# Performance work log

Hardware: AMD Instinct MI355X
Metric: run time of the kernel (lower is better)

The kernel has to match this reference:

```python
import jax, jax.numpy as jnp
import numpy as np

N_NODES = 100000


def gcn_conv(x, W, b, src, dst, n_nodes):
    """PyG-style GCNConv: h = D^{-1/2} (A + I) D^{-1/2} (x @ W) + b.

    src/dst already include self-loops. Symmetric normalization with
    degrees computed on the destination index (in-degree incl. self-loop).
    """
    h = x @ W  # [N, out] - transform before propagate (cheap gather dim)
    deg = jax.ops.segment_sum(jnp.ones_like(dst, dtype=h.dtype), dst,
                              num_segments=n_nodes)  # [N]
    dinv = jnp.where(deg > 0, jax.lax.rsqrt(deg), 0.0)  # deg^{-1/2}, 0 for isolated
    norm = dinv[src] * dinv[dst]  # [E]
    msg = h[src] * norm[:, None]  # gather + normalize, [E, out]
    out = jax.ops.segment_sum(msg, dst, num_segments=n_nodes)  # scatter-sum
    return out + b


def setup_inputs() -> dict:
    key = jax.random.key(0)
    k1, k2, k3, k4 = jax.random.split(key, 4)
    in_dim, hidden, n_edges = 128, 32, 3200000
    x = jax.random.normal(k1, (N_NODES, in_dim), dtype=jnp.float32)
    edge_index = jax.random.randint(k2, (2, n_edges), 0, N_NODES, dtype=jnp.int64)
    W1 = jax.random.normal(k3, (in_dim, hidden), dtype=jnp.float32) / np.sqrt(in_dim)
    b1 = jnp.zeros((hidden,), dtype=jnp.float32)
    W2 = jax.random.normal(k4, (hidden, 1), dtype=jnp.float32) / np.sqrt(hidden)
    b2 = jnp.zeros((1,), dtype=jnp.float32)
    return {"x": x, "edge_index": edge_index, "W1": W1, "b1": b1,
            "W2": W2, "b2": b2}


def reference(x, edge_index, W1, b1, W2, b2):
    n = x.shape[0]
    loops = jnp.arange(n, dtype=edge_index.dtype)
    src = jnp.concatenate([edge_index[0], loops])  # add self-loops
    dst = jnp.concatenate([edge_index[1], loops])
    h = jax.nn.relu(gcn_conv(x, W1, b1, src, dst, n))
    out = jax.nn.sigmoid(gcn_conv(h, W2, b2, src, dst, n))
    return out.squeeze(-1)  # [N]
```

## Files before the change

kernel.cpp:

```cpp
#include <hip/hip_runtime.h>
#include <hip/hip_bf16.h>
#include <stdint.h>

#define IN_DIM 128
#define HID 32
#define CSHIFT 8
#define CNODES 256
#define CAP 9216
#define NPART 8
#define SUBCAP 1280
#define TILE 4096
#define NBC_MAX 400

__device__ __forceinline__ float bf_lo(uint u) {
    uint t = u << 16; return *(float*)&t;
}
__device__ __forceinline__ float bf_hi(uint u) {
    uint t = u & 0xFFFF0000u; return *(float*)&t;
}

__global__ __launch_bounds__(256) void binB_kernel(const int* __restrict__ src,
                                                   const int* __restrict__ dst,
                                                   int* __restrict__ pcursor,
                                                   int* __restrict__ pbuf,
                                                   int e, int nbc) {
    __shared__ int pk[TILE];
    __shared__ short binsArr[TILE];
    __shared__ int hist[NBC_MAX];
    __shared__ int gbase[NBC_MAX];
    int part = blockIdx.x & (NPART - 1);
    int base = blockIdx.x * TILE;
    int cnt = min(TILE, e - base);
    if (cnt <= 0) return;
    for (int i = threadIdx.x; i < nbc; i += 256) hist[i] = 0;
    __syncthreads();
    for (int i = threadIdx.x; i < cnt; i += 256) {
        int s = __builtin_nontemporal_load(src + base + i);
        int d = __builtin_nontemporal_load(dst + base + i);
        int bin = d >> CSHIFT;
        pk[i] = s | ((d & (CNODES - 1)) << 17);
        binsArr[i] = (short)bin;
        atomicAdd(&hist[bin], 1);
    }
    __syncthreads();
    for (int i = threadIdx.x; i < nbc; i += 256) {
        int c = hist[i];
        gbase[i] = (c > 0) ? atomicAdd(&pcursor[part * nbc + i], c) : 0;
        hist[i] = 0;
    }
    __syncthreads();
    for (int i = threadIdx.x; i < cnt; i += 256) {
        int bin = binsArr[i];
        int slot = atomicAdd(&hist[bin], 1);
        int pos = gbase[bin] + slot;
        if (pos < SUBCAP)
            pbuf[(size_t)(part * nbc + bin) * SUBCAP + pos] = pk[i];
    }
}

__global__ __launch_bounds__(256) void sortmm_kernel(const int* __restrict__ pcursor,
                                                     const int* __restrict__ pbuf,
                                                     int* __restrict__ csr,
                                                     int* __restrict__ row_beg,
                                                     int* __restrict__ row_end,
                                                     float* __restrict__ dinv_g,
                                                     const float* __restrict__ x,
                                                     const float* __restrict__ W1,
                                                     __hip_bfloat16* __restrict__ h1s,
                                                     int n, int nbc) {
    int b = blockIdx.x;
    __shared__ int sbe[CAP];
    __shared__ int hist[CNODES];
    __shared__ int offs[CNODES];
    __shared__ int cur[CNODES];
    __shared__ int scnt[NPART + 1];
    int tid = threadIdx.x;
    if (tid == 0) {
        int run = 0;
        for (int p = 0; p < NPART; p++) {
            scnt[p] = run;
            run += min(pcursor[p * nbc + b], SUBCAP);
        }
        scnt[NPART] = run;
    }
    hist[tid] = 0;
    __syncthreads();
    for (int p = 0; p < NPART; p++) {
        int cnt = scnt[p + 1] - scnt[p];
        const int* seg = pbuf + (size_t)(p * nbc + b) * SUBCAP;
        int dstoff = scnt[p];
        for (int i = tid; i < cnt; i += 256) {
            int v = __builtin_nontemporal_load(seg + i);
            if (dstoff + i < CAP) {
                sbe[dstoff + i] = v;
                atomicAdd(&hist[v >> 17], 1);
            }
        }
    }
    __syncthreads();
    if (tid < 64) {
        int lane = tid;
        int b4 = lane * 4;
        int s0 = hist[b4], s1 = hist[b4 + 1], s2 = hist[b4 + 2], s3 = hist[b4 + 3];
        int lsum = s0 + s1 + s2 + s3;
        int pref = lsum;
#pragma unroll
        for (int m = 1; m < 64; m <<= 1) {
            int t = __shfl_up(pref, m);
            if (lane >= m) pref += t;
        }
        pref -= lsum;
        offs[b4] = pref;           cur[b4] = pref;
        offs[b4 + 1] = pref + s0;  cur[b4 + 1] = pref + s0;
        offs[b4 + 2] = pref + s0 + s1;       cur[b4 + 2] = pref + s0 + s1;
        offs[b4 + 3] = pref + s0 + s1 + s2;  cur[b4 + 3] = pref + s0 + s1 + s2;
    }
    __syncthreads();
    int total = min(scnt[NPART], CAP);
    int base = b * CAP;
    for (int i = tid; i < total; i += 256) {
        int p = sbe[i];
        int pos = atomicAdd(&cur[p >> 17], 1);
        csr[base + pos] = p & 0x1FFFF;
    }
    int node = b * CNODES + tid;
    int h = hist[tid];
    float dv = rsqrtf((float)h + 1.0f);
    if (node < n) {
        int o = offs[tid];
        row_beg[node] = base + o;
        row_end[node] = base + o + h;
        dinv_g[node] = dv;
    }
    __syncthreads();
    float* Ws = (float*)sbe;
    for (int i = tid; i < IN_DIM * HID; i += 256) Ws[i] = W1[i];
    __syncthreads();
    if (node >= n) return;
    float acc[HID];
#pragma unroll
    for (int j = 0; j < HID; j++) acc[j] = 0.f;
    const float4* xr = (const float4*)(x + (size_t)node * IN_DIM);
#pragma unroll 4
    for (int k4 = 0; k4 < IN_DIM / 4; k4++) {
        float4 xv = xr[k4];
        int k = k4 * 4;
#pragma unroll
        for (int j = 0; j < HID; j++) {
            acc[j] += xv.x * Ws[(k + 0) * HID + j] + xv.y * Ws[(k + 1) * HID + j]
                    + xv.z * Ws[(k + 2) * HID + j] + xv.w * Ws[(k + 3) * HID + j];
        }
    }
    uint pkd[16];
#pragma unroll
    for (int q = 0; q < 16; q++) {
        __hip_bfloat162 p2 = __float22bfloat162_rn(make_float2(acc[2 * q] * dv, acc[2 * q + 1] * dv));
        pkd[q] = *(uint*)&p2;
    }
    uint4* o = (uint4*)(h1s + (size_t)node * HID);
#pragma unroll
    for (int q = 0; q < 4; q++)
        o[q] = make_uint4(pkd[4 * q], pkd[4 * q + 1], pkd[4 * q + 2], pkd[4 * q + 3]);
}

__global__ __launch_bounds__(256) void gather1_kernel(const int* __restrict__ row_beg,
                                                      const int* __restrict__ row_end,
                                                      const int* __restrict__ csr,
                                                      const float* __restrict__ dinv,
                                                      const __hip_bfloat16* __restrict__ h1s,
                                                      const float* __restrict__ b1,
                                                      const float* __restrict__ W2,
                                                      float* __restrict__ h2s, int n) {
    int wave = (blockIdx.x * 256 + threadIdx.x) >> 6;
    int gwaves = (gridDim.x * 256) >> 6;
    int lane = threadIdx.x & 63;
    int j2 = lane & 15;
    int quad = lane >> 4;
    const uint* h1u = (const uint*)h1s;
    float b1a = b1[2 * j2], b1b = b1[2 * j2 + 1];
    float w2a = W2[2 * j2], w2b = W2[2 * j2 + 1];
    for (int d = wave; d < n; d += gwaves) {
        int beg = row_beg[d], end = row_end[d];
        float a0 = 0.f, a1 = 0.f;
        int p = beg + quad;
        for (; p + 12 < end; p += 16) {
            int s0 = csr[p];
            int s1 = csr[p + 4];
            int s2 = csr[p + 8];
            int s3 = csr[p + 12];
            uint u0 = h1u[(size_t)s0 * 16 + j2];
            uint u1 = h1u[(size_t)s1 * 16 + j2];
            uint u2 = h1u[(size_t)s2 * 16 + j2];
            uint u3 = h1u[(size_t)s3 * 16 + j2];
            a0 += bf_lo(u0) + bf_lo(u1) + bf_lo(u2) + bf_lo(u3);
            a1 += bf_hi(u0) + bf_hi(u1) + bf_hi(u2) + bf_hi(u3);
        }
        for (; p < end; p += 4) {
            uint u = h1u[(size_t)csr[p] * 16 + j2];
            a0 += bf_lo(u);
            a1 += bf_hi(u);
        }
        a0 += __shfl_xor(a0, 16);  a0 += __shfl_xor(a0, 32);
        a1 += __shfl_xor(a1, 16);  a1 += __shfl_xor(a1, 32);
        float dd = dinv[d];
        uint su = h1u[(size_t)d * 16 + j2];
        float v0 = (a0 + bf_lo(su)) * dd + b1a;
        float v1 = (a1 + bf_hi(su)) * dd + b1b;
        v0 = fmaxf(v0, 0.f);
        v1 = fmaxf(v1, 0.f);
        float pv = v0 * w2a + v1 * w2b;
#pragma unroll
        for (int m = 1; m < 16; m <<= 1) pv += __shfl_xor(pv, m);
        if (lane == 0) h2s[d] = pv * dd;
    }
}

__global__ __launch_bounds__(256) void gather2_kernel(const int* __restrict__ row_beg,
                                                      const int* __restrict__ row_end,
                                                      const int* __restrict__ csr,
                                                      const float* __restrict__ dinv,
                                                      const float* __restrict__ h2s,
                                                      const float* __restrict__ b2,
                                                      float* __restrict__ out, int n) {
    int hw = (blockIdx.x * 256 + threadIdx.x) >> 5;
    int ghw = (gridDim.x * 256) >> 5;
    int l = threadIdx.x & 31;
    float bias = b2[0];
    for (int d = hw; d < n; d += ghw) {
        int beg = row_beg[d], end = row_end[d];
        float acc = 0.f;
        for (int p = beg + l; p < end; p += 32) {
            acc += h2s[csr[p]];
        }
#pragma unroll
        for (int m = 1; m < 32; m <<= 1) acc += __shfl_xor(acc, m, 32);
        if (l == 0) {
            float dd = dinv[d];
            float v = (acc + h2s[d]) * dd + bias;
            out[d] = 1.f / (1.f + expf(-v));
        }
    }
}

extern "C" void kernel_launch(void* const* d_in, const int* in_sizes, int n_in,
                              void* d_out, int out_size, void* d_ws, size_t ws_size,
                              hipStream_t stream) {
    const float* x  = (const float*)d_in[0];
    const int*   ei = (const int*)d_in[1];
    const float* W1 = (const float*)d_in[2];
    const float* b1 = (const float*)d_in[3];
    const float* W2 = (const float*)d_in[4];
    const float* b2 = (const float*)d_in[5];
    float* out = (float*)d_out;

    const int n = in_sizes[0] / IN_DIM;
    const int e = in_sizes[1] / 2;
    const int* src = ei;
    const int* dst = ei + e;
    const int nbc = (n + CNODES - 1) >> CSHIFT;

    int*   pbuf    = (int*)d_ws;
    int*   csr     = pbuf + (size_t)NPART * nbc * SUBCAP;
    __hip_bfloat16* h1s = (__hip_bfloat16*)(csr + (size_t)nbc * CAP);
    float* dinv    = (float*)(h1s + (size_t)n * HID);
    float* h2s     = dinv + n;
    int*   row_beg = (int*)(h2s + n);
    int*   row_end = row_beg + n;
    int*   pcursor = row_end + n;

    const int B = 256;
    int gBin = (e + TILE - 1) / TILE;
    int gP = 2048;
    int m  = NPART * nbc;

    hipMemsetAsync(pcursor, 0, (size_t)m * sizeof(int), stream);
    binB_kernel<<<gBin, B, 0, stream>>>(src, dst, pcursor, pbuf, e, nbc);
    sortmm_kernel<<<nbc, B, 0, stream>>>(pcursor, pbuf, csr, row_beg, row_end, dinv,
                                         x, W1, h1s, n, nbc);
    gather1_kernel<<<gP, B, 0, stream>>>(row_beg, row_end, csr, dinv, h1s, b1, W2, h2s, n);
    gather2_kernel<<<gP, B, 0, stream>>>(row_beg, row_end, csr, dinv, h2s, b2, out, n);
}
```

Measured before the change: 256.0 us.

## Halve nodes per CSR block and split each node's W1 matmul across two threads

Halves the number of nodes per CSR bucket (256 to 128), with matching capacities, so twice as many blocks build CSR and the block count limit doubles. In the fused kernel each node's x@W1 is now split across a thread pair over the K dimension and combined with a lane shuffle; each thread writes half of the bf16 output row. This raises parallelism and shortens per-thread work in the dense transform, at the cost of more blocks, an extra shuffle reduction, and smaller per-bucket capacity headroom that could overflow with skewed degrees.

```diff
diff --git a/kernel.cpp b/kernel.cpp
--- a/kernel.cpp
+++ b/kernel.cpp
@@ -4,13 +4,13 @@
 
 #define IN_DIM 128
 #define HID 32
-#define CSHIFT 8
-#define CNODES 256
-#define CAP 9216
+#define CSHIFT 7
+#define CNODES 128
+#define CAP 4608
 #define NPART 8
-#define SUBCAP 1280
+#define SUBCAP 672
 #define TILE 4096
-#define NBC_MAX 400
+#define NBC_MAX 800
 
 __device__ __forceinline__ float bf_lo(uint u) {
     uint t = u << 16; return *(float*)&t;
@@ -83,7 +83,7 @@
         }
         scnt[NPART] = run;
     }
-    hist[tid] = 0;
+    if (tid < CNODES) hist[tid] = 0;
     __syncthreads();
     for (int p = 0; p < NPART; p++) {
         int cnt = scnt[p + 1] - scnt[p];
@@ -100,9 +100,9 @@
     __syncthreads();
     if (tid < 64) {
         int lane = tid;
-        int b4 = lane * 4;
-        int s0 = hist[b4], s1 = hist[b4 + 1], s2 = hist[b4 + 2], s3 = hist[b4 + 3];
-        int lsum = s0 + s1 + s2 + s3;
+        int b2 = lane * 2;
+        int s0 = hist[b2], s1 = hist[b2 + 1];
+        int lsum = s0 + s1;
         int pref = lsum;
 #pragma unroll
         for (int m = 1; m < 64; m <<= 1) {
@@ -110,10 +110,8 @@
             if (lane >= m) pref += t;
         }
         pref -= lsum;
-        offs[b4] = pref;           cur[b4] = pref;
-        offs[b4 + 1] = pref + s0;  cur[b4 + 1] = pref + s0;
-        offs[b4 + 2] = pref + s0 + s1;       cur[b4 + 2] = pref + s0 + s1;
-        offs[b4 + 3] = pref + s0 + s1 + s2;  cur[b4 + 3] = pref + s0 + s1 + s2;
+        offs[b2] = pref;           cur[b2] = pref;
+        offs[b2 + 1] = pref + s0;  cur[b2 + 1] = pref + s0;
     }
     __syncthreads();
     int total = min(scnt[NPART], CAP);
@@ -123,44 +121,51 @@
         int pos = atomicAdd(&cur[p >> 17], 1);
         csr[base + pos] = p & 0x1FFFF;
     }
-    int node = b * CNODES + tid;
-    int h = hist[tid];
-    float dv = rsqrtf((float)h + 1.0f);
-    if (node < n) {
-        int o = offs[tid];
-        row_beg[node] = base + o;
-        row_end[node] = base + o + h;
-        dinv_g[node] = dv;
+    if (tid < CNODES) {
+        int node = b * CNODES + tid;
+        if (node < n) {
+            int o = offs[tid], h = hist[tid];
+            row_beg[node] = base + o;
+            row_end[node] = base + o + h;
+            dinv_g[node] = rsqrtf((float)h + 1.0f);
+        }
     }
     __syncthreads();
     float* Ws = (float*)sbe;
     for (int i = tid; i < IN_DIM * HID; i += 256) Ws[i] = W1[i];
     __syncthreads();
-    if (node >= n) return;
+    int node2 = b * CNODES + (tid >> 1);
+    int khalf = tid & 1;
+    if (node2 >= n) return;
+    float dv = rsqrtf((float)hist[tid >> 1] + 1.0f);
     float acc[HID];
 #pragma unroll
     for (int j = 0; j < HID; j++) acc[j] = 0.f;
-    const float4* xr = (const float4*)(x + (size_t)node * IN_DIM);
+    const float4* xr = (const float4*)(x + (size_t)node2 * IN_DIM + khalf * 64);
+    int kbase = khalf * 64;
 #pragma unroll 4
-    for (int k4 = 0; k4 < IN_DIM / 4; k4++) {
+    for (int k4 = 0; k4 < 16; k4++) {
         float4 xv = xr[k4];
-        int k = k4 * 4;
+        int k = kbase + k4 * 4;
 #pragma unroll
         for (int j = 0; j < HID; j++) {
             acc[j] += xv.x * Ws[(k + 0) * HID + j] + xv.y * Ws[(k + 1) * HID + j]
                     + xv.z * Ws[(k + 2) * HID + j] + xv.w * Ws[(k + 3) * HID + j];
         }
     }
-    uint pkd[16];
-#pragma unroll
-    for (int q = 0; q < 16; q++) {
-        __hip_bfloat162 p2 = __float22bfloat162_rn(make_float2(acc[2 * q] * dv, acc[2 * q + 1] * dv));
+#pragma unroll
+    for (int j = 0; j < HID; j++) acc[j] += __shfl_xor(acc[j], 1);
+    uint pkd[8];
+    int abase = khalf * 16;
+#pragma unroll
+    for (int q = 0; q < 8; q++) {
+        __hip_bfloat162 p2 = __float22bfloat162_rn(
+            make_float2(acc[abase + 2 * q] * dv, acc[abase + 2 * q + 1] * dv));
         pkd[q] = *(uint*)&p2;
     }
-    uint4* o = (uint4*)(h1s + (size_t)node * HID);
-#pragma unroll
-    for (int q = 0; q < 4; q++)
-        o[q] = make_uint4(pkd[4 * q], pkd[4 * q + 1], pkd[4 * q + 2], pkd[4 * q + 3]);
+    uint4* o = (uint4*)(h1s + (size_t)node2 * HID) + khalf * 2;
+    o[0] = make_uint4(pkd[0], pkd[1], pkd[2], pkd[3]);
+    o[1] = make_uint4(pkd[4], pkd[5], pkd[6], pkd[7]);
 }
 
 __global__ __launch_bounds__(256) void gather1_kernel(const int* __restrict__ row_beg,
```

Result: no change. 252.4 us (-1.4%).
